# Kernel optimization log

Measured on AMD Instinct MI355X. Metric: run time of the kernel, lower is better.

## Reference

```python
import jax, jax.numpy as jnp
import numpy as np

B, C, D_EMB = 512, 100000, 128
SCALE = 3.0
EPS = 1e-5


def _l2norm(x, eps=1e-12):
    # matches torch F.normalize(p=2, dim=-1)
    n = jnp.sqrt(jnp.sum(x * x, axis=-1, keepdims=True))
    return x / jnp.maximum(n, eps)


def setup_inputs() -> dict:
    key = jax.random.key(0)
    k1, k2, k3 = jax.random.split(key, 3)
    X = jax.random.normal(k1, (B, D_EMB), dtype=jnp.float32)
    indices = jnp.arange(B, dtype=jnp.int64)
    T = jax.random.randint(k2, (B,), 0, C).astype(jnp.int64)
    proxies = jax.random.normal(k3, (C, D_EMB), dtype=jnp.float32) / 8.0
    return {"X": X, "indices": indices, "T": T, "proxies": proxies}


def reference(X, indices, T, proxies):
    P = _l2norm(proxies)            # (C, D)
    Xn = _l2norm(X)                 # (B, D)

    # cross_attention -----------------------------------------------------
    Pb = P[T]                       # (B, D) gather of class proxies
    # affinity2boundary[b,k] = relu(<(Pb[b]+Pb[k])/2, Xn[k]>)
    #   = relu(0.5 * ((Pb @ Xn.T)[b,k] + diag[k]))  -- avoids (B,B,D) intermediate
    diag = jnp.sum(Pb * Xn, axis=-1)                       # (B,)
    aff2b = jax.nn.relu(0.5 * (Pb @ Xn.T + diag[None, :]))  # (B, B)
    aff2x = jax.nn.relu(Xn @ Xn.T)                          # (B, B)
    attention = aff2b + aff2x

    # NOTE: faithful to torch broadcasting: (B,B) / (B,) divides by COLUMN sums
    attention = attention / (attention.sum(-1) + EPS)       # (B, B)
    attention_weights = attention @ Xn                      # (B, D)
    X2 = Xn + attention_weights

    Ps = SCALE * _l2norm(P)         # (C, D), rows have norm SCALE
    Xs = SCALE * _l2norm(X2)        # (B, D)

    # squared pairwise distance block between X rows and proxy rows
    sx = jnp.sum(Xs * Xs, axis=-1)  # (B,)
    sp = jnp.sum(Ps * Ps, axis=-1)  # (C,)
    Dm = jnp.maximum(sx[:, None] + sp[None, :] - 2.0 * (Xs @ Ps.T), 0.0)  # (B, C)

    # one-hot targets (smoothing_const = 0) with masked log-softmax
    lsm = jax.nn.log_softmax(-Dm, axis=-1)                  # (B, C)
    loss = -lsm[jnp.arange(B), T]                           # (B,)
    return loss.mean()
```

## Files before the change

kernel.cpp:

```cpp
#include <hip/hip_runtime.h>
#include <hip/hip_bf16.h>
#include <math.h>

#define B_N 512
#define C_N 100000
#define CPAD 100032
#define D_N 128
#define NCHUNK (CPAD / 64)
#define KP_BLOCKS (CPAD / 8)
#define K6_GX 256
#define K6_BLOCKS K6_GX
#define PAD_CORR (32.0f * 1.522998e-8f)

typedef short short8 __attribute__((ext_vector_type(8)));
typedef float f32x4 __attribute__((ext_vector_type(4)));

__device__ __forceinline__ unsigned short f2bf(float f) {
  unsigned int u = __float_as_uint(f);
  u += 0x7fffu + ((u >> 16) & 1u);
  return (unsigned short)(u >> 16);
}

__device__ __forceinline__ void gl_lds16(const void* g, void* l) {
  __builtin_amdgcn_global_load_lds(
      (const __attribute__((address_space(1))) void*)g,
      (__attribute__((address_space(3))) void*)l, 16, 0, 0);
}

template <int NT>
__device__ __forceinline__ float block_reduce_sum(float v, float* red) {
  int t = threadIdx.x;
  __syncthreads();
  red[t] = v;
  __syncthreads();
#pragma unroll
  for (int s = NT / 2; s > 0; s >>= 1) {
    if (t < s) red[t] += red[t + s];
    __syncthreads();
  }
  return red[0];
}

__global__ __launch_bounds__(256) void kA(const float* __restrict__ X,
                                          const float* __restrict__ proxies,
                                          const int* __restrict__ T,
                                          float* __restrict__ Xn, float* __restrict__ Pb,
                                          float* __restrict__ diagv,
                                          unsigned short* __restrict__ Pnb,
                                          int* __restrict__ ctrs) {
  int bid = blockIdx.x;
  int t = threadIdx.x;
  if (bid < KP_BLOCKS) {
    int w = t >> 6, lane = t & 63;
    int half = lane >> 5, l32 = lane & 31;
    int row = bid * 8 + w * 2 + half;
    float4 v = make_float4(0.f, 0.f, 0.f, 0.f);
    if (row < C_N) v = *(const float4*)(proxies + (size_t)row * D_N + 4 * l32);
    float ss = v.x * v.x + v.y * v.y + v.z * v.z + v.w * v.w;
#pragma unroll
    for (int off = 1; off < 32; off <<= 1) ss += __shfl_xor(ss, off);
    float inv = 1.f / fmaxf(sqrtf(ss), 1e-12f);
    unsigned int p0 = (unsigned int)f2bf(v.x * inv) | ((unsigned int)f2bf(v.y * inv) << 16);
    unsigned int p1 = (unsigned int)f2bf(v.z * inv) | ((unsigned int)f2bf(v.w * inv) << 16);
    *(uint2*)(Pnb + (size_t)row * D_N + 4 * l32) = make_uint2(p0, p1);
  } else {
    __shared__ float red[256];
    int b = bid - KP_BLOCKS;
    bool act = t < D_N;
    float v = act ? X[b * D_N + t] : 0.f;
    float ss = block_reduce_sum<256>(v * v, red);
    float xn = v / fmaxf(sqrtf(ss), 1e-12f);
    if (act) Xn[b * D_N + t] = xn;
    int row = T[b];
    float p = act ? proxies[(size_t)row * D_N + t] : 0.f;
    float ss2 = block_reduce_sum<256>(p * p, red);
    float pn = p / fmaxf(sqrtf(ss2), 1e-12f);
    if (act) Pb[b * D_N + t] = pn;
    float d = block_reduce_sum<256>(pn * xn, red);
    if (t == 0) {
      diagv[b] = d;
      if (b == 0) ctrs[32] = 0;
    }
  }
}

__global__ __launch_bounds__(512) void k3_att(const float* __restrict__ Xn,
                                              const float* __restrict__ Pb,
                                              const float* __restrict__ diagv,
                                              float* __restrict__ A, float* __restrict__ S) {
  __shared__ float xb[128], pbv[128];
  __shared__ float red[512];
  int b = blockIdx.x, t = threadIdx.x;
  if (t < 128) {
    xb[t] = Xn[b * D_N + t];
    pbv[t] = Pb[b * D_N + t];
  }
  __syncthreads();
  const float4* xr = (const float4*)(Xn + (size_t)t * D_N);
  float d1 = 0.f, d2 = 0.f;
#pragma unroll
  for (int i = 0; i < 32; i++) {
    float4 v = xr[i];
    d1 += pbv[4 * i] * v.x + pbv[4 * i + 1] * v.y + pbv[4 * i + 2] * v.z + pbv[4 * i + 3] * v.w;
    d2 += xb[4 * i] * v.x + xb[4 * i + 1] * v.y + xb[4 * i + 2] * v.z + xb[4 * i + 3] * v.w;
  }
  float a = fmaxf(0.5f * (d1 + diagv[t]), 0.f) + fmaxf(d2, 0.f);
  A[(size_t)b * B_N + t] = a;
  float rs = block_reduce_sum<512>(a, red);
  if (t == 0) S[b] = rs;
}

__global__ __launch_bounds__(512) void k4ab(const float* __restrict__ Xn,
                                            const float* __restrict__ Pb,
                                            const float* __restrict__ A,
                                            const float* __restrict__ S,
                                            unsigned short* __restrict__ Xsb,
                                            float* __restrict__ lossT,
                                            float* __restrict__ sumexpP) {
  __shared__ float xb[128], pbv[128];
  __shared__ float aw[512];
  __shared__ float red[512];
  int b = blockIdx.x, t = threadIdx.x;
  if (t < 128) {
    xb[t] = Xn[b * D_N + t];
    pbv[t] = Pb[b * D_N + t];
  }
  aw[t] = A[(size_t)b * B_N + t] / (S[t] + 1e-5f);
  __syncthreads();

  int d = t & 127, h = t >> 7;
  const float* xp = Xn + (size_t)(128 * h) * D_N + d;
  const float* awp = aw + 128 * h;
  float a0 = 0.f, a1 = 0.f, a2 = 0.f, a3 = 0.f;
#pragma unroll 8
  for (int kk = 0; kk < 128; kk += 4) {
    a0 = fmaf(awp[kk], xp[(size_t)kk * D_N], a0);
    a1 = fmaf(awp[kk + 1], xp[(size_t)(kk + 1) * D_N], a1);
    a2 = fmaf(awp[kk + 2], xp[(size_t)(kk + 2) * D_N], a2);
    a3 = fmaf(awp[kk + 3], xp[(size_t)(kk + 3) * D_N], a3);
  }
  red[t] = (a0 + a1) + (a2 + a3);
  __syncthreads();
  float x2 = (t < 128) ? (xb[t] + red[t] + red[t + 128] + red[t + 256] + red[t + 384]) : 0.f;

  float ss = block_reduce_sum<512>(x2 * x2, red);
  float xs = 3.f * x2 / fmaxf(sqrtf(ss), 1e-12f);
  if (t < 128) Xsb[b * D_N + t] = f2bf(xs);
  float dt = block_reduce_sum<512>((t < 128) ? xs * pbv[t] : 0.f, red);
  if (t == 0) {
    lossT[b] = fmaxf(18.f - 6.f * dt, 0.f);
    sumexpP[b * 16] = 0.f;
  }
}

__global__ __launch_bounds__(512, 2) void k6_big(const unsigned short* __restrict__ Pnb,
                                                 const unsigned short* __restrict__ Xsb,
                                                 float* __restrict__ sumexpP,
                                                 const float* __restrict__ lossT,
                                                 int* __restrict__ ctrs,
                                                 float* __restrict__ out) {
  __shared__ __align__(16) unsigned short sP[2][64 * 128];
  __shared__ float redf[512];
  __shared__ int sLast;
  const int t = threadIdx.x;
  const int w = t >> 6;
  const int lane = t & 63;
  const int lc = lane & 15;
  const int q = lane >> 4;

  short8 afr[4][4];
#pragma unroll
  for (int mt = 0; mt < 4; mt++)
#pragma unroll
    for (int ks = 0; ks < 4; ks++)
      afr[mt][ks] = *(const short8*)(Xsb + (size_t)(64 * w + 16 * mt + lc) * D_N +
                                     ks * 32 + q * 8);

  float pe[4][4];
#pragma unroll
  for (int mt = 0; mt < 4; mt++)
#pragma unroll
    for (int r = 0; r < 4; r++) pe[mt][r] = 0.f;

  const int rR = 8 * w + (lane >> 4);
  const int gsrc0 = (lane & 15);
#define STAGE(c0_, buf_)                                                              \
  {                                                                                   \
    _Pragma("unroll") for (int j = 0; j < 2; j++) {                                   \
      int R = rR + 4 * j;                                                             \
      int g = gsrc0 ^ ((R)&15);                                                       \
      gl_lds16(Pnb + (((size_t)(c0_) + R) << 7) + (g << 3),                           \
               &sP[buf_][w * 1024 + j * 512]);                                        \
    }                                                                                 \
  }

  int cc = blockIdx.x;
  STAGE(cc * 64, 0);
  int buf = 0;
  while (true) {
    int nc = cc + gridDim.x;
    if (nc < NCHUNK) {
      STAGE(nc * 64, buf ^ 1);
      __builtin_amdgcn_sched_barrier(0);
      __builtin_amdgcn_s_waitcnt(0x0F72);
    } else {
      __builtin_amdgcn_sched_barrier(0);
      __builtin_amdgcn_s_waitcnt(0x0F70);
    }
    __builtin_amdgcn_s_barrier();
    __builtin_amdgcn_sched_barrier(0);

    f32x4 acc[4][4];
#pragma unroll
    for (int mt = 0; mt < 4; mt++)
#pragma unroll
      for (int nt = 0; nt < 4; nt++) acc[mt][nt] = (f32x4){0.f, 0.f, 0.f, 0.f};

#pragma unroll
    for (int ks = 0; ks < 4; ks++) {
      short8 bfr[4];
#pragma unroll
      for (int nt = 0; nt < 4; nt++) {
        int R = 16 * nt + lc;
        int g = (ks * 4 + q) ^ lc;
        bfr[nt] = *(const short8*)(&sP[buf][R * 128 + (g << 3)]);
      }
#pragma unroll
      for (int nt = 0; nt < 4; nt++)
#pragma unroll
        for (int mt = 0; mt < 4; mt++)
          acc[mt][nt] = __builtin_amdgcn_mfma_f32_16x16x32_bf16(afr[mt][ks], bfr[nt],
                                                                acc[mt][nt], 0, 0, 0);
    }

#pragma unroll
    for (int mt = 0; mt < 4; mt++)
#pragma unroll
      for (int nt = 0; nt < 4; nt++) {
        f32x4 a = acc[mt][nt];
#pragma unroll
        for (int r = 0; r < 4; r++)
          pe[mt][r] += __builtin_amdgcn_exp2f(
              fminf(__fmaf_rn(8.65617024533378f, a[r], -25.9685107360013f), 0.f));
      }

    if (nc >= NCHUNK) break;
    __builtin_amdgcn_sched_barrier(0);
    __builtin_amdgcn_s_barrier();
    cc = nc;
    buf ^= 1;
  }

#pragma unroll
  for (int mt = 0; mt < 4; mt++) {
#pragma unroll
    for (int r = 0; r < 4; r++) {
      float p = pe[mt][r];
      p += __shfl_xor(p, 1);
      p += __shfl_xor(p, 2);
      p += __shfl_xor(p, 4);
      p += __shfl_xor(p, 8);
      if (lc == 0) {
        int rb = 64 * w + 16 * mt + 4 * q + r;
        atomicAdd(&sumexpP[rb * 16], p);
      }
    }
  }

  __builtin_amdgcn_s_waitcnt(0);
  if (t == 0) sLast = atomicAdd(&ctrs[32], 1);
  __syncthreads();
  if (sLast == K6_BLOCKS - 1) {
    float se = __hip_atomic_load(&sumexpP[t * 16], __ATOMIC_RELAXED,
                                 __HIP_MEMORY_SCOPE_AGENT);
    float v = lossT[t] + logf(se - PAD_CORR);
    float s = block_reduce_sum<512>(v, redf);
    if (t == 0) out[0] = s * (1.0f / 512.0f);
  }
}

extern "C" void kernel_launch(void* const* d_in, const int* in_sizes, int n_in,
                              void* d_out, int out_size, void* d_ws, size_t ws_size,
                              hipStream_t stream) {
  const float* X = (const float*)d_in[0];
  const int* T = (const int*)d_in[2];
  const float* proxies = (const float*)d_in[3];
  float* out = (float*)d_out;

  char* ws = (char*)d_ws;
  unsigned short* Pnb = (unsigned short*)ws;
  float* Xn = (float*)(ws + (size_t)CPAD * D_N * 2);
  float* Pb = Xn + B_N * D_N;
  float* X2 = Pb + B_N * D_N;
  float* dg = X2 + B_N * D_N;
  float* S = dg + B_N;
  float* lossT = S + B_N;
  float* sumexpP = lossT + B_N;
  unsigned short* Xsb = (unsigned short*)(sumexpP + B_N * 16);
  float* A = (float*)(Xsb + B_N * D_N);
  int* ctrs = (int*)(A + B_N * B_N);

  kA<<<KP_BLOCKS + B_N, 256, 0, stream>>>(X, proxies, T, Xn, Pb, dg, Pnb, ctrs);
  k3_att<<<B_N, 512, 0, stream>>>(Xn, Pb, dg, A, S);
  k4ab<<<B_N, 512, 0, stream>>>(Xn, Pb, A, S, Xsb, lossT, sumexpP);
  k6_big<<<K6_GX, 512, 0, stream>>>(Pnb, Xsb, sumexpP, lossT, ctrs, out);
}
```

Baseline: 151.3 us.

## Fuse proxy normalization and bf16 conversion into the main distance kernel

Removes the separate pass that normalizes all proxies and writes a bf16 copy to workspace. The big MFMA kernel now streams raw fp32 proxy rows into LDS, computes row norms, converts to bf16 and writes a swizzled single-buffered tile before the matmul. This saves one full write and reread of the proxy matrix. In exchange it loads twice as many bytes per chunk inside the hot kernel and needs much more LDS (two fp32 tiles), which may lower occupancy and adds a conversion step on the critical path of every chunk.

```diff
diff --git a/kernel.cpp b/kernel.cpp
--- a/kernel.cpp
+++ b/kernel.cpp
@@ -7,7 +7,6 @@
 #define CPAD 100032
 #define D_N 128
 #define NCHUNK (CPAD / 64)
-#define KP_BLOCKS (CPAD / 8)
 #define K6_GX 256
 #define K6_BLOCKS K6_GX
 #define PAD_CORR (32.0f * 1.522998e-8f)
@@ -21,6 +20,10 @@
   return (unsigned short)(u >> 16);
 }
 
+__device__ __forceinline__ unsigned int pk2bf(float lo, float hi) {
+  return (unsigned int)f2bf(lo) | ((unsigned int)f2bf(hi) << 16);
+}
+
 __device__ __forceinline__ void gl_lds16(const void* g, void* l) {
   __builtin_amdgcn_global_load_lds(
       (const __attribute__((address_space(1))) void*)g,
@@ -41,46 +44,29 @@
   return red[0];
 }
 
-__global__ __launch_bounds__(256) void kA(const float* __restrict__ X,
+__global__ __launch_bounds__(256) void kX(const float* __restrict__ X,
                                           const float* __restrict__ proxies,
                                           const int* __restrict__ T,
                                           float* __restrict__ Xn, float* __restrict__ Pb,
                                           float* __restrict__ diagv,
-                                          unsigned short* __restrict__ Pnb,
                                           int* __restrict__ ctrs) {
-  int bid = blockIdx.x;
+  __shared__ float red[256];
+  int b = blockIdx.x;
   int t = threadIdx.x;
-  if (bid < KP_BLOCKS) {
-    int w = t >> 6, lane = t & 63;
-    int half = lane >> 5, l32 = lane & 31;
-    int row = bid * 8 + w * 2 + half;
-    float4 v = make_float4(0.f, 0.f, 0.f, 0.f);
-    if (row < C_N) v = *(const float4*)(proxies + (size_t)row * D_N + 4 * l32);
-    float ss = v.x * v.x + v.y * v.y + v.z * v.z + v.w * v.w;
-#pragma unroll
-    for (int off = 1; off < 32; off <<= 1) ss += __shfl_xor(ss, off);
-    float inv = 1.f / fmaxf(sqrtf(ss), 1e-12f);
-    unsigned int p0 = (unsigned int)f2bf(v.x * inv) | ((unsigned int)f2bf(v.y * inv) << 16);
-    unsigned int p1 = (unsigned int)f2bf(v.z * inv) | ((unsigned int)f2bf(v.w * inv) << 16);
-    *(uint2*)(Pnb + (size_t)row * D_N + 4 * l32) = make_uint2(p0, p1);
-  } else {
-    __shared__ float red[256];
-    int b = bid - KP_BLOCKS;
-    bool act = t < D_N;
-    float v = act ? X[b * D_N + t] : 0.f;
-    float ss = block_reduce_sum<256>(v * v, red);
-    float xn = v / fmaxf(sqrtf(ss), 1e-12f);
-    if (act) Xn[b * D_N + t] = xn;
-    int row = T[b];
-    float p = act ? proxies[(size_t)row * D_N + t] : 0.f;
-    float ss2 = block_reduce_sum<256>(p * p, red);
-    float pn = p / fmaxf(sqrtf(ss2), 1e-12f);
-    if (act) Pb[b * D_N + t] = pn;
-    float d = block_reduce_sum<256>(pn * xn, red);
-    if (t == 0) {
-      diagv[b] = d;
-      if (b == 0) ctrs[32] = 0;
-    }
+  bool act = t < D_N;
+  float v = act ? X[b * D_N + t] : 0.f;
+  float ss = block_reduce_sum<256>(v * v, red);
+  float xn = v / fmaxf(sqrtf(ss), 1e-12f);
+  if (act) Xn[b * D_N + t] = xn;
+  int row = T[b];
+  float p = act ? proxies[(size_t)row * D_N + t] : 0.f;
+  float ss2 = block_reduce_sum<256>(p * p, red);
+  float pn = p / fmaxf(sqrtf(ss2), 1e-12f);
+  if (act) Pb[b * D_N + t] = pn;
+  float d = block_reduce_sum<256>(pn * xn, red);
+  if (t == 0) {
+    diagv[b] = d;
+    if (b == 0) ctrs[32] = 0;
   }
 }
 
@@ -153,13 +139,14 @@
   }
 }
 
-__global__ __launch_bounds__(512, 2) void k6_big(const unsigned short* __restrict__ Pnb,
+__global__ __launch_bounds__(512, 2) void k6_big(const float* __restrict__ proxies,
                                                  const unsigned short* __restrict__ Xsb,
                                                  float* __restrict__ sumexpP,
                                                  const float* __restrict__ lossT,
                                                  int* __restrict__ ctrs,
                                                  float* __restrict__ out) {
-  __shared__ __align__(16) unsigned short sP[2][64 * 128];
+  __shared__ __align__(16) float fP[2][64 * 128];
+  __shared__ __align__(16) unsigned short sP[64 * 128];
   __shared__ float redf[512];
   __shared__ int sLast;
   const int t = threadIdx.x;
@@ -182,31 +169,67 @@
 #pragma unroll
     for (int r = 0; r < 4; r++) pe[mt][r] = 0.f;
 
-  const int rR = 8 * w + (lane >> 4);
-  const int gsrc0 = (lane & 15);
-#define STAGE(c0_, buf_)                                                              \
+  const int srow = 8 * w + (lane >> 5);
+  const int scol = (lane & 31) * 4;
+#define STAGEF(c0_, buf_)                                                             \
   {                                                                                   \
-    _Pragma("unroll") for (int j = 0; j < 2; j++) {                                   \
-      int R = rR + 4 * j;                                                             \
-      int g = gsrc0 ^ ((R)&15);                                                       \
-      gl_lds16(Pnb + (((size_t)(c0_) + R) << 7) + (g << 3),                           \
-               &sP[buf_][w * 1024 + j * 512]);                                        \
+    _Pragma("unroll") for (int j = 0; j < 4; j++) {                                   \
+      int gr = (c0_) + srow + 2 * j;                                                  \
+      gr = gr < C_N ? gr : (C_N - 1);               \
+      gl_lds16(proxies + (size_t)gr * D_N + scol,                                     \
+               &fP[buf_][(8 * w + 2 * j) * D_N]);                                     \
     }                                                                                 \
   }
 
+  const int cr = t >> 3;
+  const int cs = t & 7;
+
   int cc = blockIdx.x;
-  STAGE(cc * 64, 0);
+  STAGEF(cc * 64, 0);
   int buf = 0;
   while (true) {
     int nc = cc + gridDim.x;
     if (nc < NCHUNK) {
-      STAGE(nc * 64, buf ^ 1);
+      STAGEF(nc * 64, buf ^ 1);
       __builtin_amdgcn_sched_barrier(0);
-      __builtin_amdgcn_s_waitcnt(0x0F72);
+      __builtin_amdgcn_s_waitcnt(0x0F74);
     } else {
       __builtin_amdgcn_sched_barrier(0);
       __builtin_amdgcn_s_waitcnt(0x0F70);
     }
+    __builtin_amdgcn_sched_barrier(0);
+
+    {
+      const float* src = &fP[buf][cr * D_N + cs * 16];
+      float4 v0 = ((const float4*)src)[0];
+      float4 v1 = ((const float4*)src)[1];
+      float4 v2 = ((const float4*)src)[2];
+      float4 v3 = ((const float4*)src)[3];
+      float s0 = v0.x * v0.x + v0.y * v0.y + v0.z * v0.z + v0.w * v0.w;
+      float s1 = v1.x * v1.x + v1.y * v1.y + v1.z * v1.z + v1.w * v1.w;
+      float s2 = v2.x * v2.x + v2.y * v2.y + v2.z * v2.z + v2.w * v2.w;
+      float s3 = v3.x * v3.x + v3.y * v3.y + v3.z * v3.z + v3.w * v3.w;
+      float ss = (s0 + s1) + (s2 + s3);
+      ss += __shfl_xor(ss, 1);
+      ss += __shfl_xor(ss, 2);
+      ss += __shfl_xor(ss, 4);
+      float inv = 1.f / fmaxf(sqrtf(ss), 1e-12f);
+      if (cc * 64 + cr >= C_N) inv = 0.f;
+      uint4 g0, g1;
+      g0.x = pk2bf(v0.x * inv, v0.y * inv);
+      g0.y = pk2bf(v0.z * inv, v0.w * inv);
+      g0.z = pk2bf(v1.x * inv, v1.y * inv);
+      g0.w = pk2bf(v1.z * inv, v1.w * inv);
+      g1.x = pk2bf(v2.x * inv, v2.y * inv);
+      g1.y = pk2bf(v2.z * inv, v2.w * inv);
+      g1.z = pk2bf(v3.x * inv, v3.y * inv);
+      g1.w = pk2bf(v3.z * inv, v3.w * inv);
+      int P0 = (2 * cs) ^ (cr & 15);
+      int P1 = (2 * cs + 1) ^ (cr & 15);
+      *(uint4*)&sP[cr * D_N + P0 * 8] = g0;
+      *(uint4*)&sP[cr * D_N + P1 * 8] = g1;
+    }
+    __builtin_amdgcn_s_waitcnt(0xC07F);
     __builtin_amdgcn_s_barrier();
     __builtin_amdgcn_sched_barrier(0);
 
@@ -223,7 +246,7 @@
       for (int nt = 0; nt < 4; nt++) {
         int R = 16 * nt + lc;
         int g = (ks * 4 + q) ^ lc;
-        bfr[nt] = *(const short8*)(&sP[buf][R * 128 + (g << 3)]);
+        bfr[nt] = *(const short8*)(&sP[R * 128 + (g << 3)]);
       }
 #pragma unroll
       for (int nt = 0; nt < 4; nt++)
@@ -288,7 +311,6 @@
   float* out = (float*)d_out;
 
   char* ws = (char*)d_ws;
-  unsigned short* Pnb = (unsigned short*)ws;
   float* Xn = (float*)(ws + (size_t)CPAD * D_N * 2);
   float* Pb = Xn + B_N * D_N;
   float* X2 = Pb + B_N * D_N;
@@ -300,8 +322,8 @@
   float* A = (float*)(Xsb + B_N * D_N);
   int* ctrs = (int*)(A + B_N * B_N);
 
-  kA<<<KP_BLOCKS + B_N, 256, 0, stream>>>(X, proxies, T, Xn, Pb, dg, Pnb, ctrs);
+  kX<<<B_N, 256, 0, stream>>>(X, proxies, T, Xn, Pb, dg, ctrs);
   k3_att<<<B_N, 512, 0, stream>>>(Xn, Pb, dg, A, S);
   k4ab<<<B_N, 512, 0, stream>>>(Xn, Pb, A, S, Xsb, lossT, sumexpP);
-  k6_big<<<K6_GX, 512, 0, stream>>>(Pnb, Xsb, sumexpP, lossT, ctrs, out);
-}
+  k6_big<<<K6_GX, 512, 0, stream>>>(proxies, Xsb, sumexpP, lossT, ctrs, out);
+}
```

Result: faster. 142.3 us (-6.0%).
